# Kernel optimization log

Measured on AMD Instinct MI355X. Metric: run time of the kernel, lower is better.

## Reference

```python
import jax, jax.numpy as jnp
import numpy as np

B, MAX_H, MAX_W, D, S, HID = 64, 64, 32, 512, 8, 64


def setup_inputs() -> dict:
    key = jax.random.key(0)
    ks = jax.random.split(key, 7)
    return {
        "canonical": jax.random.normal(ks[0], (S, S, D), jnp.float32) * 0.02,
        "w1": jax.random.normal(ks[1], (2, HID), jnp.float32) * 0.5,
        "b1": jax.random.normal(ks[2], (HID,), jnp.float32) * 0.1,
        "w2": jax.random.normal(ks[3], (HID, D), jnp.float32) * 0.05,
        "b2": jax.random.normal(ks[4], (D,), jnp.float32) * 0.05,
        "batch_size": B,
        "target_h_list": jax.random.randint(ks[5], (B,), 1, MAX_H + 1, jnp.int32),
        "target_w_list": jax.random.randint(ks[6], (B,), 1, MAX_W + 1, jnp.int32),
        "max_h": MAX_H,
        "max_w": MAX_W,
    }


def _axis_coords(sizes, max_len):
    # sizes: [B] clamped lengths; returns normalized coords u in [0,1] at each
    # padded position (torch.linspace(0,1,L) semantics; 0 when L==1). [B, max_len]
    idx = jnp.arange(max_len, dtype=jnp.float32)[None, :]
    L = sizes[:, None].astype(jnp.float32)
    return jnp.where(L > 1, idx / jnp.maximum(L - 1.0, 1.0), 0.0)


def _forward(canonical, w1, b1, w2, b2, target_h_list, target_w_list, max_h, max_w):
    S_ = canonical.shape[0]
    Hs = jnp.clip(target_h_list, 1, max_h)  # [B]
    Ws = jnp.clip(target_w_list, 1, max_w)  # [B]

    u = _axis_coords(Hs, max_h)  # [B, mh]
    v = _axis_coords(Ws, max_w)  # [B, mw]

    # Bilinear resize of canonical grid with align_corners=True:
    # source coord = normalized coord * (S-1)
    sy = jnp.clip(u * (S_ - 1), 0.0, S_ - 1.0)  # [B, mh]
    sx = jnp.clip(v * (S_ - 1), 0.0, S_ - 1.0)  # [B, mw]
    y0 = jnp.floor(sy).astype(jnp.int32)
    x0 = jnp.floor(sx).astype(jnp.int32)
    y1 = jnp.minimum(y0 + 1, S_ - 1)
    x1 = jnp.minimum(x0 + 1, S_ - 1)
    wy = (sy - y0.astype(jnp.float32))[:, :, None, None]  # [B, mh, 1, 1]
    wx = (sx - x0.astype(jnp.float32))[:, None, :, None]  # [B, 1, mw, 1]

    yi0 = y0[:, :, None]  # [B, mh, 1]
    yi1 = y1[:, :, None]
    xi0 = x0[:, None, :]  # [B, 1, mw]
    xi1 = x1[:, None, :]
    q00 = canonical[yi0, xi0]  # [B, mh, mw, D]
    q01 = canonical[yi0, xi1]
    q10 = canonical[yi1, xi0]
    q11 = canonical[yi1, xi1]
    bil = ((1.0 - wy) * ((1.0 - wx) * q00 + wx * q01)
           + wy * ((1.0 - wx) * q10 + wx * q11))  # [B, mh, mw, D]

    # Coordinate refinement MLP on (u, v)
    coords = jnp.stack(
        [jnp.broadcast_to(u[:, :, None], (u.shape[0], max_h, max_w)),
         jnp.broadcast_to(v[:, None, :], (u.shape[0], max_h, max_w))],
        axis=-1)  # [B, mh, mw, 2]
    h = jax.nn.gelu(coords @ w1 + b1, approximate=False)
    delta = h @ w2 + b2  # [B, mh, mw, D]

    mask = ((jnp.arange(max_h)[None, :, None] < Hs[:, None, None])
            & (jnp.arange(max_w)[None, None, :] < Ws[:, None, None]))  # [B, mh, mw]
    queries = jnp.where(mask[..., None], bil + delta, 0.0)
    return queries, mask


def reference(canonical, w1, b1, w2, b2, batch_size, target_h_list,
              target_w_list, max_h, max_w):
    return _forward(canonical, w1, b1, w2, b2, target_h_list, target_w_list,
                    max_h, max_w)
```

## Files before the change

kernel.cpp:

```cpp
#include <hip/hip_runtime.h>
#include <math.h>

#define NB    64
#define MAXH  64
#define MAXW  32
#define DCH   512
#define SS    8
#define HID   64

#define QTOTAL ((size_t)NB * MAXH * MAXW * DCH)

typedef float f4  __attribute__((ext_vector_type(4)));
typedef short s8v __attribute__((ext_vector_type(8)));

__device__ __forceinline__ float gelu_exact(float x) {
    return 0.5f * x * (1.0f + erff(x * 0.70710678118654752440f));
}

__device__ __forceinline__ unsigned short bf16_rne(float x) {
    unsigned int u = __float_as_uint(x);
    unsigned int r = u + 0x7fffu + ((u >> 16) & 1u);
    return (unsigned short)(r >> 16);
}

__global__ __launch_bounds__(256) void w2prep_kernel(
    const float* __restrict__ w2, s8v* __restrict__ w2b)
{
    const int tid  = blockIdx.x * 256 + threadIdx.x;
    const int lane = tid & 63;
    const int ct   = (tid >> 6) & 31;
    const int kh   = tid >> 11;
    const int q    = lane >> 4;
    const int m    = lane & 15;
    const int c    = ct * 16 + m;
    union { s8v v; unsigned short us[8]; } pk;
    #pragma unroll
    for (int j = 0; j < 8; ++j) {
        const int k = kh * 32 + q * 8 + j;
        pk.us[j] = bf16_rne(w2[k * DCH + c]);
    }
    w2b[tid] = pk.v;
}

__global__ __launch_bounds__(256) void hgqg_kernel(
    const float* __restrict__ canonical,
    const float* __restrict__ w1,
    const float* __restrict__ b1,
    const s8v*   __restrict__ w2b,
    const float* __restrict__ b2,
    const int*   __restrict__ hlist,
    const int*   __restrict__ wlist,
    float* __restrict__ out)
{
    const int raw  = blockIdx.x;
    const int id   = (raw ^ (raw >> 7)) & 8191;
    const int i    = id & 63;
    const int half = (id >> 6) & 1;
    const int b    = id >> 7;
    const int blk  = (b << 6) | i;
    const int t    = threadIdx.x;

    int H = hlist[b]; H = min(max(H, 1), MAXH);
    int W = wlist[b]; W = min(max(W, 1), MAXW);

    const int jbase = half << 4;

    f4* q4 = (f4*)(out + (size_t)blk * (MAXW * DCH)) + jbase * 128;

    if (half == 0 && t < MAXW) {
        out[QTOTAL + (size_t)blk * MAXW + t] = (i < H && t < W) ? 1.0f : 0.0f;
    }

    const f4 z = {0.f, 0.f, 0.f, 0.f};

    if (i >= H || jbase >= W) {
        #pragma unroll
        for (int r = 0; r < 8; ++r) q4[t + r * 256] = z;
        return;
    }

    const float u    = (H > 1) ? (float)i / (float)(H - 1) : 0.0f;
    const float sy   = fminf(u * 7.0f, 7.0f);
    const int   y0   = (int)sy;
    const int   y1   = min(y0 + 1, SS - 1);
    const float wy   = sy - (float)y0;
    const float winv = (W > 1) ? 1.0f / (float)(W - 1) : 0.0f;

    __shared__ __align__(16) float ri[SS * 516];
    {
        const f4* can4 = (const f4*)canonical;
        #pragma unroll
        for (int rr = 0; rr < 4; ++rr) {
            const int idx = t + rr * 256;
            const int x   = idx >> 7;
            const int c4  = idx & 127;
            const f4 a = can4[(y0 * SS + x) * 128 + c4];
            const f4 d = can4[(y1 * SS + x) * 128 + c4];
            *(f4*)&ri[x * 516 + c4 * 4] = a + wy * (d - a);
        }
    }

    __shared__ __align__(16) float hsh[16][68];
    {
        const int jl = t >> 4;
        const int k0 = (t & 15) * 4;
        const float v = (float)(jbase + jl) * winv;
        #pragma unroll
        for (int kk = 0; kk < 4; ++kk) {
            const int k = k0 + kk;
            hsh[jl][k] = gelu_exact(u * w1[k] + v * w1[HID + k] + b1[k]);
        }
    }
    __syncthreads();

    const int l = t & 63;
    const int w = t >> 6;
    const int q = l >> 4;
    const int m = l & 15;

    union { s8v v; unsigned short us[8]; } A0, A1;
    {
        const float* hrow = &hsh[m][q * 8];
        #pragma unroll
        for (int j = 0; j < 8; ++j) {
            A0.us[j] = bf16_rne(hrow[j]);
            A1.us[j] = bf16_rne(hrow[32 + j]);
        }
    }

    int   x0a[4], x1a[4];
    float wxa[4];
    #pragma unroll
    for (int r = 0; r < 4; ++r) {
        const int   j  = jbase + q * 4 + r;
        const float v  = (float)j * winv;
        const float sx = fminf(v * 7.0f, 7.0f);
        const int   x0 = (int)sx;
        x0a[r] = x0;
        x1a[r] = min(x0 + 1, SS - 1);
        wxa[r] = sx - (float)x0;
    }

    const size_t obase = (size_t)blk * (MAXW * DCH) + (size_t)jbase * DCH;

    #pragma unroll
    for (int tt = 0; tt < 8; ++tt) {
        const int ct = w * 8 + tt;
        const int c  = ct * 16 + m;

        f4 acc;
        const float bb2 = b2[c];
        #pragma unroll
        for (int r = 0; r < 4; ++r) {
            const float f0 = ri[x0a[r] * 516 + c];
            const float f1 = ri[x1a[r] * 516 + c];
            acc[r] = f0 + wxa[r] * (f1 - f0) + bb2;
        }

        const s8v b0 = w2b[ct * 64 + l];
        const s8v b1f = w2b[2048 + ct * 64 + l];
        acc = __builtin_amdgcn_mfma_f32_16x16x32_bf16(A0.v, b0, acc, 0, 0, 0);
        acc = __builtin_amdgcn_mfma_f32_16x16x32_bf16(A1.v, b1f, acc, 0, 0, 0);

        #pragma unroll
        for (int r = 0; r < 4; ++r) {
            const int j = jbase + q * 4 + r;
            out[obase + (size_t)(q * 4 + r) * DCH + c] = (j < W) ? acc[r] : 0.0f;
        }
    }
}

extern "C" void kernel_launch(void* const* d_in, const int* in_sizes, int n_in,
                              void* d_out, int out_size, void* d_ws, size_t ws_size,
                              hipStream_t stream) {
    const float* canonical = (const float*)d_in[0];
    const float* w1        = (const float*)d_in[1];
    const float* b1        = (const float*)d_in[2];
    const float* w2        = (const float*)d_in[3];
    const float* b2        = (const float*)d_in[4];
    const int*   hlist     = (const int*)d_in[6];
    const int*   wlist     = (const int*)d_in[7];
    float* out = (float*)d_out;
    s8v*   w2b = (s8v*)d_ws;

    w2prep_kernel<<<16, 256, 0, stream>>>(w2, w2b);
    hgqg_kernel<<<2 * NB * MAXH, 256, 0, stream>>>(
        canonical, w1, b1, w2b, b2, hlist, wlist, out);
}
```

Before: 280.9 us.

## Fold horizontal bilinear interpolation into an extra bf16 MFMA

The x-direction bilinear blend is now expressed as a matrix multiply. The y-interpolated canonical row is stored in shared memory as packed bf16 (8 x-positions per channel), and a sparse weight vector per output column is accumulated through a third MFMA instead of scalar shared-memory gathers. This removes the fp32 staging buffer and per-element lerp arithmetic. It also adds a fast path that drops the per-element mask select when the whole half-row is valid. The cost is bf16 rounding of the interpolated canonical values and weights, which lowers accuracy, plus an extra MFMA per tile.

```diff
diff --git a/kernel.cpp b/kernel.cpp
--- a/kernel.cpp
+++ b/kernel.cpp
@@ -86,18 +86,18 @@
     const float wy   = sy - (float)y0;
     const float winv = (W > 1) ? 1.0f / (float)(W - 1) : 0.0f;
 
-    __shared__ __align__(16) float ri[SS * 516];
-    {
-        const f4* can4 = (const f4*)canonical;
-        #pragma unroll
-        for (int rr = 0; rr < 4; ++rr) {
-            const int idx = t + rr * 256;
-            const int x   = idx >> 7;
-            const int c4  = idx & 127;
-            const f4 a = can4[(y0 * SS + x) * 128 + c4];
-            const f4 d = can4[(y1 * SS + x) * 128 + c4];
-            *(f4*)&ri[x * 516 + c4 * 4] = a + wy * (d - a);
-        }
+    __shared__ __align__(16) s8v extb[512];
+    #pragma unroll
+    for (int ee = 0; ee < 2; ++ee) {
+        const int e = t + ee * 256;
+        union { s8v v; unsigned short us[8]; } pk;
+        #pragma unroll
+        for (int x = 0; x < 8; ++x) {
+            const float a = canonical[(y0 * SS + x) * DCH + e];
+            const float d = canonical[(y1 * SS + x) * DCH + e];
+            pk.us[x] = bf16_rne(a + wy * (d - a));
+        }
+        extb[e] = pk.v;
     }
 
     __shared__ __align__(16) float hsh[16][68];
@@ -128,44 +128,55 @@
         }
     }
 
-    int   x0a[4], x1a[4];
-    float wxa[4];
-    #pragma unroll
-    for (int r = 0; r < 4; ++r) {
-        const int   j  = jbase + q * 4 + r;
-        const float v  = (float)j * winv;
+    union { s8v v; unsigned short us[8]; } Ax;
+    {
+        float wloc[8];
+        #pragma unroll
+        for (int x = 0; x < 8; ++x) wloc[x] = 0.0f;
+        const float v  = (float)(jbase + m) * winv;
         const float sx = fminf(v * 7.0f, 7.0f);
         const int   x0 = (int)sx;
-        x0a[r] = x0;
-        x1a[r] = min(x0 + 1, SS - 1);
-        wxa[r] = sx - (float)x0;
-    }
-
+        const int   x1 = min(x0 + 1, SS - 1);
+        const float wx = sx - (float)x0;
+        wloc[x0] += 1.0f - wx;
+        wloc[x1] += wx;
+        #pragma unroll
+        for (int x = 0; x < 8; ++x)
+            Ax.us[x] = (q == 0) ? bf16_rne(wloc[x]) : (unsigned short)0;
+    }
+
+    const bool fullhalf = (jbase + 16 <= W);
     const size_t obase = (size_t)blk * (MAXW * DCH) + (size_t)jbase * DCH;
+    const s8v zs = {0, 0, 0, 0, 0, 0, 0, 0};
 
     #pragma unroll
     for (int tt = 0; tt < 8; ++tt) {
         const int ct = w * 8 + tt;
         const int c  = ct * 16 + m;
 
+        const float bb2 = b2[c];
         f4 acc;
-        const float bb2 = b2[c];
-        #pragma unroll
-        for (int r = 0; r < 4; ++r) {
-            const float f0 = ri[x0a[r] * 516 + c];
-            const float f1 = ri[x1a[r] * 516 + c];
-            acc[r] = f0 + wxa[r] * (f1 - f0) + bb2;
-        }
-
-        const s8v b0 = w2b[ct * 64 + l];
+        acc[0] = bb2; acc[1] = bb2; acc[2] = bb2; acc[3] = bb2;
+
+        const s8v b0  = w2b[ct * 64 + l];
         const s8v b1f = w2b[2048 + ct * 64 + l];
-        acc = __builtin_amdgcn_mfma_f32_16x16x32_bf16(A0.v, b0, acc, 0, 0, 0);
+        s8v be = zs;
+        if (q == 0) be = extb[c];
+
+        acc = __builtin_amdgcn_mfma_f32_16x16x32_bf16(A0.v, b0,  acc, 0, 0, 0);
         acc = __builtin_amdgcn_mfma_f32_16x16x32_bf16(A1.v, b1f, acc, 0, 0, 0);
-
-        #pragma unroll
-        for (int r = 0; r < 4; ++r) {
-            const int j = jbase + q * 4 + r;
-            out[obase + (size_t)(q * 4 + r) * DCH + c] = (j < W) ? acc[r] : 0.0f;
+        acc = __builtin_amdgcn_mfma_f32_16x16x32_bf16(Ax.v, be,  acc, 0, 0, 0);
+
+        if (fullhalf) {
+            #pragma unroll
+            for (int r = 0; r < 4; ++r)
+                out[obase + (size_t)(q * 4 + r) * DCH + c] = acc[r];
+        } else {
+            #pragma unroll
+            for (int r = 0; r < 4; ++r) {
+                const int j = jbase + q * 4 + r;
+                out[obase + (size_t)(q * 4 + r) * DCH + c] = (j < W) ? acc[r] : 0.0f;
+            }
         }
     }
 }
```

Result: no change. 281.5 us (+0.2%).

## Make kernel persistent, fold w2 bf16 prep into register-resident fragments

Applied to the files above, without the earlier changes.

Removes the separate w2 conversion kernel. Each block now loads and converts its w2 slice into bf16 MFMA fragments in registers once. The grid shrinks from 8192 to 1024 blocks, each looping over 8 work items, so the w2 load is amortised over those items and a launch is saved. A fast path skips per-row masking when the whole half-row is valid. In exchange it raises register pressure (16 fragment vectors), which may lower occupancy, and adds per-iteration syncs that reduce latency hiding on this store-bound kernel.

```diff
diff --git a/kernel.cpp b/kernel.cpp
--- a/kernel.cpp
+++ b/kernel.cpp
@@ -23,149 +23,153 @@
     return (unsigned short)(r >> 16);
 }
 
-__global__ __launch_bounds__(256) void w2prep_kernel(
-    const float* __restrict__ w2, s8v* __restrict__ w2b)
-{
-    const int tid  = blockIdx.x * 256 + threadIdx.x;
-    const int lane = tid & 63;
-    const int ct   = (tid >> 6) & 31;
-    const int kh   = tid >> 11;
-    const int q    = lane >> 4;
-    const int m    = lane & 15;
-    const int c    = ct * 16 + m;
-    union { s8v v; unsigned short us[8]; } pk;
-    #pragma unroll
-    for (int j = 0; j < 8; ++j) {
-        const int k = kh * 32 + q * 8 + j;
-        pk.us[j] = bf16_rne(w2[k * DCH + c]);
-    }
-    w2b[tid] = pk.v;
-}
-
 __global__ __launch_bounds__(256) void hgqg_kernel(
     const float* __restrict__ canonical,
     const float* __restrict__ w1,
     const float* __restrict__ b1,
-    const s8v*   __restrict__ w2b,
+    const float* __restrict__ w2,
     const float* __restrict__ b2,
     const int*   __restrict__ hlist,
     const int*   __restrict__ wlist,
     float* __restrict__ out)
 {
-    const int raw  = blockIdx.x;
-    const int id   = (raw ^ (raw >> 7)) & 8191;
-    const int i    = id & 63;
-    const int half = (id >> 6) & 1;
-    const int b    = id >> 7;
-    const int blk  = (b << 6) | i;
-    const int t    = threadIdx.x;
-
-    int H = hlist[b]; H = min(max(H, 1), MAXH);
-    int W = wlist[b]; W = min(max(W, 1), MAXW);
-
-    const int jbase = half << 4;
-
-    f4* q4 = (f4*)(out + (size_t)blk * (MAXW * DCH)) + jbase * 128;
-
-    if (half == 0 && t < MAXW) {
-        out[QTOTAL + (size_t)blk * MAXW + t] = (i < H && t < W) ? 1.0f : 0.0f;
-    }
-
-    const f4 z = {0.f, 0.f, 0.f, 0.f};
-
-    if (i >= H || jbase >= W) {
-        #pragma unroll
-        for (int r = 0; r < 8; ++r) q4[t + r * 256] = z;
-        return;
-    }
-
-    const float u    = (H > 1) ? (float)i / (float)(H - 1) : 0.0f;
-    const float sy   = fminf(u * 7.0f, 7.0f);
-    const int   y0   = (int)sy;
-    const int   y1   = min(y0 + 1, SS - 1);
-    const float wy   = sy - (float)y0;
-    const float winv = (W > 1) ? 1.0f / (float)(W - 1) : 0.0f;
-
-    __shared__ __align__(16) float ri[SS * 516];
-    {
-        const f4* can4 = (const f4*)canonical;
-        #pragma unroll
-        for (int rr = 0; rr < 4; ++rr) {
-            const int idx = t + rr * 256;
-            const int x   = idx >> 7;
-            const int c4  = idx & 127;
-            const f4 a = can4[(y0 * SS + x) * 128 + c4];
-            const f4 d = can4[(y1 * SS + x) * 128 + c4];
-            *(f4*)&ri[x * 516 + c4 * 4] = a + wy * (d - a);
-        }
-    }
-
-    __shared__ __align__(16) float hsh[16][68];
-    {
-        const int jl = t >> 4;
-        const int k0 = (t & 15) * 4;
-        const float v = (float)(jbase + jl) * winv;
-        #pragma unroll
-        for (int kk = 0; kk < 4; ++kk) {
-            const int k = k0 + kk;
-            hsh[jl][k] = gelu_exact(u * w1[k] + v * w1[HID + k] + b1[k]);
-        }
-    }
-    __syncthreads();
-
+    const int t = threadIdx.x;
     const int l = t & 63;
     const int w = t >> 6;
     const int q = l >> 4;
     const int m = l & 15;
 
-    union { s8v v; unsigned short us[8]; } A0, A1;
-    {
-        const float* hrow = &hsh[m][q * 8];
-        #pragma unroll
-        for (int j = 0; j < 8; ++j) {
-            A0.us[j] = bf16_rne(hrow[j]);
-            A1.us[j] = bf16_rne(hrow[32 + j]);
-        }
-    }
-
-    int   x0a[4], x1a[4];
-    float wxa[4];
-    #pragma unroll
-    for (int r = 0; r < 4; ++r) {
-        const int   j  = jbase + q * 4 + r;
-        const float v  = (float)j * winv;
-        const float sx = fminf(v * 7.0f, 7.0f);
-        const int   x0 = (int)sx;
-        x0a[r] = x0;
-        x1a[r] = min(x0 + 1, SS - 1);
-        wxa[r] = sx - (float)x0;
-    }
-
-    const size_t obase = (size_t)blk * (MAXW * DCH) + (size_t)jbase * DCH;
-
+    s8v  wfrag[16];
+    float bb2[8];
     #pragma unroll
     for (int tt = 0; tt < 8; ++tt) {
         const int ct = w * 8 + tt;
         const int c  = ct * 16 + m;
+        bb2[tt] = b2[c];
+        #pragma unroll
+        for (int kh = 0; kh < 2; ++kh) {
+            union { s8v v; unsigned short us[8]; } pk;
+            #pragma unroll
+            for (int j = 0; j < 8; ++j) {
+                const int k = kh * 32 + q * 8 + j;
+                pk.us[j] = bf16_rne(w2[k * DCH + c]);
+            }
+            wfrag[tt * 2 + kh] = pk.v;
+        }
+    }
 
-        f4 acc;
-        const float bb2 = b2[c];
+    __shared__ __align__(16) float ri[SS * 516];
+    __shared__ __align__(16) float hsh[16][68];
+
+    const f4 z = {0.f, 0.f, 0.f, 0.f};
+
+    #pragma unroll 1
+    for (int it = 0; it < 8; ++it) {
+        const int raw  = (it << 10) | blockIdx.x;
+        const int id   = (raw ^ (raw >> 7)) & 8191;
+        const int i    = id & 63;
+        const int half = (id >> 6) & 1;
+        const int b    = id >> 7;
+        const int blk  = (b << 6) | i;
+
+        int H = hlist[b]; H = min(max(H, 1), MAXH);
+        int W = wlist[b]; W = min(max(W, 1), MAXW);
+        const int jbase = half << 4;
+
+        f4* q4 = (f4*)(out + (size_t)blk * (MAXW * DCH)) + jbase * 128;
+
+        if (half == 0 && t < MAXW) {
+            out[QTOTAL + (size_t)blk * MAXW + t] = (i < H && t < W) ? 1.0f : 0.0f;
+        }
+
+        if (i >= H || jbase >= W) {
+            #pragma unroll
+            for (int r = 0; r < 8; ++r) q4[t + r * 256] = z;
+            continue;
+        }
+
+        const float u    = (H > 1) ? (float)i / (float)(H - 1) : 0.0f;
+        const float sy   = fminf(u * 7.0f, 7.0f);
+        const int   y0   = (int)sy;
+        const int   y1   = min(y0 + 1, SS - 1);
+        const float wy   = sy - (float)y0;
+        const float winv = (W > 1) ? 1.0f / (float)(W - 1) : 0.0f;
+
+        __syncthreads();
+        {
+            const f4* can4 = (const f4*)canonical;
+            #pragma unroll
+            for (int rr = 0; rr < 4; ++rr) {
+                const int idx2 = t + rr * 256;
+                const int x    = idx2 >> 7;
+                const int c4   = idx2 & 127;
+                const f4 a = can4[(y0 * SS + x) * 128 + c4];
+                const f4 d = can4[(y1 * SS + x) * 128 + c4];
+                *(f4*)&ri[x * 516 + c4 * 4] = a + wy * (d - a);
+            }
+            const int jl = t >> 4;
+            const int k0 = (t & 15) * 4;
+            const float v = (float)(jbase + jl) * winv;
+            #pragma unroll
+            for (int kk = 0; kk < 4; ++kk) {
+                const int k = k0 + kk;
+                hsh[jl][k] = gelu_exact(u * w1[k] + v * w1[HID + k] + b1[k]);
+            }
+        }
+        __syncthreads();
+
+        union { s8v v; unsigned short us[8]; } A0, A1;
+        {
+            const float* hrow = &hsh[m][q * 8];
+            #pragma unroll
+            for (int j = 0; j < 8; ++j) {
+                A0.us[j] = bf16_rne(hrow[j]);
+                A1.us[j] = bf16_rne(hrow[32 + j]);
+            }
+        }
+
+        int   x0a[4], x1a[4];
+        float wxa[4];
         #pragma unroll
         for (int r = 0; r < 4; ++r) {
-            const float f0 = ri[x0a[r] * 516 + c];
-            const float f1 = ri[x1a[r] * 516 + c];
-            acc[r] = f0 + wxa[r] * (f1 - f0) + bb2;
+            const int   j  = jbase + q * 4 + r;
+            const float v  = (float)j * winv;
+            const float sx = fminf(v * 7.0f, 7.0f);
+            const int   x0 = (int)sx;
+            x0a[r] = x0;
+            x1a[r] = min(x0 + 1, SS - 1);
+            wxa[r] = sx - (float)x0;
         }
 
-        const s8v b0 = w2b[ct * 64 + l];
-        const s8v b1f = w2b[2048 + ct * 64 + l];
-        acc = __builtin_amdgcn_mfma_f32_16x16x32_bf16(A0.v, b0, acc, 0, 0, 0);
-        acc = __builtin_amdgcn_mfma_f32_16x16x32_bf16(A1.v, b1f, acc, 0, 0, 0);
+        const bool fullhalf = (jbase + 16 <= W);
+        const size_t obase = (size_t)blk * (MAXW * DCH) + (size_t)jbase * DCH;
 
         #pragma unroll
-        for (int r = 0; r < 4; ++r) {
-            const int j = jbase + q * 4 + r;
-            out[obase + (size_t)(q * 4 + r) * DCH + c] = (j < W) ? acc[r] : 0.0f;
+        for (int tt = 0; tt < 8; ++tt) {
+            const int c = (w * 8 + tt) * 16 + m;
+
+            f4 acc;
+            #pragma unroll
+            for (int r = 0; r < 4; ++r) {
+                const float f0 = ri[x0a[r] * 516 + c];
+                const float f1 = ri[x1a[r] * 516 + c];
+                acc[r] = f0 + wxa[r] * (f1 - f0) + bb2[tt];
+            }
+
+            acc = __builtin_amdgcn_mfma_f32_16x16x32_bf16(A0.v, wfrag[tt * 2 + 0], acc, 0, 0, 0);
+            acc = __builtin_amdgcn_mfma_f32_16x16x32_bf16(A1.v, wfrag[tt * 2 + 1], acc, 0, 0, 0);
+
+            if (fullhalf) {
+                #pragma unroll
+                for (int r = 0; r < 4; ++r)
+                    out[obase + (size_t)(q * 4 + r) * DCH + c] = acc[r];
+            } else {
+                #pragma unroll
+                for (int r = 0; r < 4; ++r) {
+                    const int j = jbase + q * 4 + r;
+                    out[obase + (size_t)(q * 4 + r) * DCH + c] = (j < W) ? acc[r] : 0.0f;
+                }
+            }
         }
     }
 }
@@ -181,9 +185,7 @@
     const int*   hlist     = (const int*)d_in[6];
     const int*   wlist     = (const int*)d_in[7];
     float* out = (float*)d_out;
-    s8v*   w2b = (s8v*)d_ws;
 
-    w2prep_kernel<<<16, 256, 0, stream>>>(w2, w2b);
-    hgqg_kernel<<<2 * NB * MAXH, 256, 0, stream>>>(
-        canonical, w1, b1, w2b, b2, hlist, wlist, out);
+    hgqg_kernel<<<1024, 256, 0, stream>>>(
+        canonical, w1, b1, w2, b2, hlist, wlist, out);
 }
```

Result: no change. 286.2 us (+1.9%).
